# Optimization experiments

Hardware: AMD Instinct MI355X
Metric: run time of the kernel (lower is better)

Reference implementation:

```python
import jax, jax.numpy as jnp
import numpy as np

E = 256
H_HEADS = 8
HD = E // H_HEADS
NEG = -1e9


def setup_inputs() -> dict:
    key = jax.random.key(0)
    ks = jax.random.split(key, 16)
    B, Q, Hh, Ww = 16, 100, 64, 64
    S = Hh * Ww
    std = 1.0 / np.sqrt(E)
    inp = {
        "query_features": jax.random.normal(ks[0], (B, Q, E), jnp.float32),
        "image_features": jax.random.normal(ks[1], (B, E, Hh, Ww), jnp.float32),
        "mask": jax.random.randint(ks[2], (B, Q, Hh, Ww), 0, 2) > 0,
        "pos_query_embeddings": jax.random.normal(ks[3], (B, Q, E), jnp.float32),
        "pos_image_embeddings": jax.random.normal(ks[4], (B, S, E), jnp.float32),
        "Wq": jax.random.normal(ks[5], (E, E), jnp.float32) * std,
        "bq": jnp.zeros((E,), jnp.float32),
        "Wk": jax.random.normal(ks[6], (E, E), jnp.float32) * std,
        "bk": jnp.zeros((E,), jnp.float32),
        "Wv": jax.random.normal(ks[7], (E, E), jnp.float32) * std,
        "bv": jnp.zeros((E,), jnp.float32),
        "Wo": jax.random.normal(ks[8], (E, E), jnp.float32) * std,
        "bo": jnp.zeros((E,), jnp.float32),
    }
    return inp


def reference(query_features, image_features, mask, pos_query_embeddings,
              pos_image_embeddings, Wq, bq, Wk, bk, Wv, bv, Wo, bo):
    B, _, Hh, Ww = image_features.shape
    Q = query_features.shape[1]
    S = Hh * Ww
    # (B, S, E)
    img = jnp.transpose(image_features.reshape(B, E, S), (0, 2, 1))
    q = (query_features + pos_query_embeddings) @ Wq.T + bq  # (B,Q,E)
    k = (img + pos_image_embeddings) @ Wk.T + bk              # (B,S,E)
    v = img @ Wv.T + bv                                       # (B,S,E)
    q = q.reshape(B, Q, H_HEADS, HD).transpose(0, 2, 1, 3)    # (B,H,Q,D)
    k = k.reshape(B, S, H_HEADS, HD).transpose(0, 2, 1, 3)    # (B,H,S,D)
    v = v.reshape(B, S, H_HEADS, HD).transpose(0, 2, 1, 3)
    scale = 1.0 / jnp.sqrt(jnp.asarray(HD, q.dtype))
    scores = jnp.einsum('bhqd,bhsd->bhqs', q, k) * scale
    amask = mask.reshape(B, 1, Q, S)
    scores = jnp.where(amask, scores, NEG)
    attn = jax.nn.softmax(scores, axis=-1)
    out = jnp.einsum('bhqs,bhsd->bhqd', attn, v)
    out = out.transpose(0, 2, 1, 3).reshape(B, Q, E)
    return out @ Wo.T + bo
```

## Files before the change

### kernel.cpp

```cpp
#include <hip/hip_runtime.h>
#include <math.h>

#define BB 16
#define QQ 100
#define EE 256
#define NH 8
#define HD 32
#define SS 4096
#define QP 128
#define NZ 8
#define SCHUNK (SS / NZ)
#define M0 8.0f

typedef _Float16 half8_t __attribute__((ext_vector_type(8)));
typedef _Float16 half4_t __attribute__((ext_vector_type(4)));
typedef float floatx4 __attribute__((ext_vector_type(4)));

__global__ __launch_bounds__(256) void maskpack_kernel(
    const int* __restrict__ mask, unsigned* __restrict__ mbits)
{
    int gid  = blockIdx.x * 256 + threadIdx.x;
    int lane = gid & 63;
    int F    = gid & ~63;
    int s    = (F & (SS - 1)) + lane;
    int qp   = (F >> 12) & (QP - 1);
    int b    = F >> 19;
    int qc   = min(qp, QQ - 1);
    int v    = mask[((size_t)(b * QQ + qc)) * SS + s];
    unsigned long long bal = __ballot(v != 0);
    int w = (F & (SS - 1)) >> 5;
    if (lane == 0)
        mbits[((size_t)(b * (SS / 32) + w)) * QP + qp] = (unsigned)bal;
    if (lane == 32)
        mbits[((size_t)(b * (SS / 32) + w + 1)) * QP + qp] = (unsigned)(bal >> 32);
}

__global__ __launch_bounds__(256) void wcvt_kernel(
    const float* __restrict__ Wk, const float* __restrict__ Wv,
    _Float16* __restrict__ wk16a, _Float16* __restrict__ wv16a)
{
    int gid = blockIdx.x * 256 + threadIdx.x;
    int m = gid & 8191;
    const float* src = (gid < 8192) ? Wk : Wv;
    _Float16* dst = (gid < 8192) ? wk16a : wv16a;
    int li = m & 15, gg = (m >> 4) & 3, jj = (m >> 6) & 1;
    int kk = (m >> 7) & 7, w = (m >> 10) & 7;
    int e = w * 32 + jj * 16 + li;
    int f0 = kk * 32 + gg * 8;
    float4 a0 = *(const float4*)&src[(size_t)e * EE + f0];
    float4 a1 = *(const float4*)&src[(size_t)e * EE + f0 + 4];
    half8_t h;
    h[0]=(_Float16)a0.x; h[1]=(_Float16)a0.y; h[2]=(_Float16)a0.z; h[3]=(_Float16)a0.w;
    h[4]=(_Float16)a1.x; h[5]=(_Float16)a1.y; h[6]=(_Float16)a1.z; h[7]=(_Float16)a1.w;
    *(half8_t*)&dst[(size_t)m * 8] = h;
}

#define KV_STEP(KK, PC, PN, AKC, AVC)                                        \
  {                                                                          \
    float pv0 = PC[l * 33 + w4 + 0];                                         \
    float pv1 = PC[l * 33 + w4 + 1];                                         \
    float pv2 = PC[l * 33 + w4 + 2];                                         \
    float pv3 = PC[l * 33 + w4 + 3];                                         \
    half4_t hk, hv;                                                          \
    hv[0] = (_Float16)iv0; hk[0] = (_Float16)(iv0 + pv0);                    \
    hv[1] = (_Float16)iv1; hk[1] = (_Float16)(iv1 + pv1);                    \
    hv[2] = (_Float16)iv2; hk[2] = (_Float16)(iv2 + pv2);                    \
    hv[3] = (_Float16)iv3; hk[3] = (_Float16)(iv3 + pv3);                    \
    *(half4_t*)&AVC[l * 40 + w4] = hv;                                       \
    *(half4_t*)&AKC[l * 40 + w4] = hk;                                       \
    if ((KK) < 7) {                                                          \
      PN[pr * 33 + pc4 + 0] = pg.x;                                          \
      PN[pr * 33 + pc4 + 1] = pg.y;                                          \
      PN[pr * 33 + pc4 + 2] = pg.z;                                          \
      PN[pr * 33 + pc4 + 3] = pg.w;                                          \
    }                                                                        \
    __syncthreads();                                                         \
    if ((KK) < 6) pg = *(const float4*)(posb + ((KK) + 2) * 32);             \
    if ((KK) < 7) {                                                          \
      iv0 = imgb[(size_t)(((KK) + 1) * 32 + w4 + 0) * SS];                   \
      iv1 = imgb[(size_t)(((KK) + 1) * 32 + w4 + 1) * SS];                   \
      iv2 = imgb[(size_t)(((KK) + 1) * 32 + w4 + 2) * SS];                   \
      iv3 = imgb[(size_t)(((KK) + 1) * 32 + w4 + 3) * SS];                   \
    }                                                                        \
    half8_t wk0 = *(const half8_t*)(wkb + (KK) * 1024);                      \
    half8_t wk1 = *(const half8_t*)(wkb + (KK) * 1024 + 512);                \
    half8_t wv0 = *(const half8_t*)(wvb + (KK) * 1024);                      \
    half8_t wv1 = *(const half8_t*)(wvb + (KK) * 1024 + 512);                \
    half8_t afk0 = *(const half8_t*)&AKC[(0 * 16 + li) * 40 + gg * 8];       \
    half8_t afk1 = *(const half8_t*)&AKC[(1 * 16 + li) * 40 + gg * 8];       \
    half8_t afk2 = *(const half8_t*)&AKC[(2 * 16 + li) * 40 + gg * 8];       \
    half8_t afk3 = *(const half8_t*)&AKC[(3 * 16 + li) * 40 + gg * 8];       \
    acck[0][0] = __builtin_amdgcn_mfma_f32_16x16x32_f16(afk0, wk0, acck[0][0], 0, 0, 0); \
    acck[0][1] = __builtin_amdgcn_mfma_f32_16x16x32_f16(afk0, wk1, acck[0][1], 0, 0, 0); \
    acck[1][0] = __builtin_amdgcn_mfma_f32_16x16x32_f16(afk1, wk0, acck[1][0], 0, 0, 0); \
    acck[1][1] = __builtin_amdgcn_mfma_f32_16x16x32_f16(afk1, wk1, acck[1][1], 0, 0, 0); \
    acck[2][0] = __builtin_amdgcn_mfma_f32_16x16x32_f16(afk2, wk0, acck[2][0], 0, 0, 0); \
    acck[2][1] = __builtin_amdgcn_mfma_f32_16x16x32_f16(afk2, wk1, acck[2][1], 0, 0, 0); \
    acck[3][0] = __builtin_amdgcn_mfma_f32_16x16x32_f16(afk3, wk0, acck[3][0], 0, 0, 0); \
    acck[3][1] = __builtin_amdgcn_mfma_f32_16x16x32_f16(afk3, wk1, acck[3][1], 0, 0, 0); \
    half8_t afv0 = *(const half8_t*)&AVC[(0 * 16 + li) * 40 + gg * 8];       \
    half8_t afv1 = *(const half8_t*)&AVC[(1 * 16 + li) * 40 + gg * 8];       \
    half8_t afv2 = *(const half8_t*)&AVC[(2 * 16 + li) * 40 + gg * 8];       \
    half8_t afv3 = *(const half8_t*)&AVC[(3 * 16 + li) * 40 + gg * 8];       \
    accv[0][0] = __builtin_amdgcn_mfma_f32_16x16x32_f16(afv0, wv0, accv[0][0], 0, 0, 0); \
    accv[0][1] = __builtin_amdgcn_mfma_f32_16x16x32_f16(afv0, wv1, accv[0][1], 0, 0, 0); \
    accv[1][0] = __builtin_amdgcn_mfma_f32_16x16x32_f16(afv1, wv0, accv[1][0], 0, 0, 0); \
    accv[1][1] = __builtin_amdgcn_mfma_f32_16x16x32_f16(afv1, wv1, accv[1][1], 0, 0, 0); \
    accv[2][0] = __builtin_amdgcn_mfma_f32_16x16x32_f16(afv2, wv0, accv[2][0], 0, 0, 0); \
    accv[2][1] = __builtin_amdgcn_mfma_f32_16x16x32_f16(afv2, wv1, accv[2][1], 0, 0, 0); \
    accv[3][0] = __builtin_amdgcn_mfma_f32_16x16x32_f16(afv3, wv0, accv[3][0], 0, 0, 0); \
    accv[3][1] = __builtin_amdgcn_mfma_f32_16x16x32_f16(afv3, wv1, accv[3][1], 0, 0, 0); \
  }

__global__ __launch_bounds__(512, 2) void fused_kv_kernel(
    const float* __restrict__ img,
    const float* __restrict__ pos,
    const _Float16* __restrict__ wk16a, const float* __restrict__ bk,
    const _Float16* __restrict__ wv16a, const float* __restrict__ bv,
    _Float16* __restrict__ kbuf,
    _Float16* __restrict__ vt)
{
    __shared__ __align__(16) char smem_raw[37376];
    float* posT0 = (float*)smem_raw;
    float* posT1 = posT0 + 64 * 33;
    _Float16* A0k = (_Float16*)(posT1 + 64 * 33);
    _Float16* A0v = A0k + 2560;
    _Float16* A1k = A0v + 2560;
    _Float16* A1v = A1k + 2560;

    const int t  = threadIdx.x;
    const int w  = t >> 6, l = t & 63;
    const int gg = l >> 4, li = l & 15;
    const int pr = t >> 3, pc = t & 7;
    const int w4 = w * 4, pc4 = pc * 4;

    const int m0 = blockIdx.x * 64;
    const int b  = m0 >> 12;
    const int s0 = m0 & (SS - 1);

    const float* imgb = img + (size_t)b * EE * SS + s0 + l;
    const float* posb = pos + ((size_t)(b * SS + s0 + pr)) * EE + pc4;
    const _Float16* wkb = wk16a + ((size_t)(w * 16) * 64 + l) * 8;
    const _Float16* wvb = wv16a + ((size_t)(w * 16) * 64 + l) * 8;

    floatx4 acck[4][2] = {};
    floatx4 accv[4][2] = {};

    float4 pg = *(const float4*)posb;
    float iv0 = imgb[(size_t)(w4 + 0) * SS];
    float iv1 = imgb[(size_t)(w4 + 1) * SS];
    float iv2 = imgb[(size_t)(w4 + 2) * SS];
    float iv3 = imgb[(size_t)(w4 + 3) * SS];
    posT0[pr * 33 + pc4 + 0] = pg.x;
    posT0[pr * 33 + pc4 + 1] = pg.y;
    posT0[pr * 33 + pc4 + 2] = pg.z;
    posT0[pr * 33 + pc4 + 3] = pg.w;
    pg = *(const float4*)(posb + 32);
    __syncthreads();

    #pragma unroll 1
    for (int kp = 0; kp < 4; ++kp) {
        const int kk = kp * 2;
        KV_STEP(kk,     posT0, posT1, A0k, A0v)
        KV_STEP(kk + 1, posT1, posT0, A1k, A1v)
    }

    #pragma unroll
    for (int jj = 0; jj < 2; ++jj) {
        int e = w * 32 + jj * 16 + li;
        float bj = bk[e];
        #pragma unroll
        for (int i = 0; i < 4; ++i) {
            int row = m0 + i * 16 + gg * 4;
            #pragma unroll
            for (int r = 0; r < 4; ++r)
                kbuf[(size_t)(row + r) * EE + e] = (_Float16)(acck[i][jj][r] + bj);
        }
    }

    __syncthreads();
    _Float16* vstage = (_Float16*)smem_raw;
    #pragma unroll
    for (int jj = 0; jj < 2; ++jj) {
        int e_loc = w * 32 + jj * 16 + li;
        float bj = bv[e_loc];
        #pragma unroll
        for (int i = 0; i < 4; ++i) {
            int s_loc = i * 16 + gg * 4;
            half4_t h4;
            #pragma unroll
            for (int r = 0; r < 4; ++r)
                h4[r] = (_Float16)(accv[i][jj][r] + bj);
            *(half4_t*)&vstage[e_loc * 72 + s_loc] = h4;
        }
    }
    __syncthreads();
    #pragma unroll
    for (int c = 0; c < 4; ++c) {
        int row = c * 64 + (t >> 3);
        int so  = (t & 7) * 8;
        half8_t v8 = *(const half8_t*)&vstage[row * 72 + so];
        int hh = row >> 5, dd = row & 31;
        *(half8_t*)(vt + ((size_t)((b * NH + hh) * HD + dd)) * SS + s0 + so) = v8;
    }
}

__global__ __launch_bounds__(256) void proj_kernel(
    const float* __restrict__ x1, const float* __restrict__ x2,
    const float* __restrict__ W, const float* __restrict__ bias,
    float* __restrict__ outf, _Float16* __restrict__ out16,
    float oscale, int has_x2)
{
    const int row0 = blockIdx.x * 8;
    const int t = threadIdx.x;
    __shared__ float xs[8][256];

    #pragma unroll
    for (int p = 0; p < 8; ++p) {
        int idx = t + p * 256;
        int f = idx & 255, j = idx >> 8;
        size_t g = (size_t)(row0 + j) * EE + f;
        float v = x1[g];
        if (has_x2) v += x2[g];
        xs[j][f] = v;
    }
    __syncthreads();

    const int e = t;
    const float* wrow = W + (size_t)e * EE;
    float acc[8];
    const float bv = bias[e];
    #pragma unroll
    for (int j = 0; j < 8; ++j) acc[j] = bv;

    #pragma unroll 4
    for (int f4 = 0; f4 < 64; ++f4) {
        float4 w4 = *(const float4*)(wrow + f4 * 4);
        #pragma unroll
        for (int j = 0; j < 8; ++j) {
            float4 x4 = *(const float4*)&xs[j][f4 * 4];
            acc[j] = fmaf(w4.x, x4.x, acc[j]);
            acc[j] = fmaf(w4.y, x4.y, acc[j]);
            acc[j] = fmaf(w4.z, x4.z, acc[j]);
            acc[j] = fmaf(w4.w, x4.w, acc[j]);
        }
    }
    if (out16) {
        #pragma unroll
        for (int j = 0; j < 8; ++j)
            out16[(size_t)(row0 + j) * EE + e] = (_Float16)(acc[j] * oscale);
    } else {
        #pragma unroll
        for (int j = 0; j < 8; ++j)
            outf[(size_t)(row0 + j) * EE + e] = acc[j];
    }
}

__global__ __launch_bounds__(256) void attn_mfma_kernel(
    const _Float16* __restrict__ q16,
    const _Float16* __restrict__ kbuf,
    const _Float16* __restrict__ vt,
    const unsigned* __restrict__ mbits,
    float* __restrict__ part,
    float* __restrict__ pl)
{
    const int z = blockIdx.x, h = blockIdx.y, b = blockIdx.z;
    const int t = threadIdx.x;
    const int w = t >> 6, l = t & 63;
    const int g = l >> 4, li = l & 15;

    __shared__ _Float16 ks[64 * 40];
    __shared__ _Float16 vs[32 * 72];
    __shared__ _Float16 ps[128 * 72];
    __shared__ unsigned mw[2][QP];

    half8_t qf[2];
    {
        int q0r = min(32 * w + li, QQ - 1);
        int q1r = min(32 * w + 16 + li, QQ - 1);
        qf[0] = *(const half8_t*)(q16 + ((size_t)(b * QQ + q0r)) * EE + h * HD + g * 8);
        qf[1] = *(const half8_t*)(q16 + ((size_t)(b * QQ + q1r)) * EE + h * HD + g * 8);
    }

    float lsum[2][4] = {{0.f}};
    floatx4 accO[2][2] = {};

    for (int it = 0; it < SCHUNK / 64; ++it) {
        const int sblk = z * SCHUNK + it * 64;

        {
            int sl = t >> 2, koff = (t & 3) * 8;
            *(half8_t*)&ks[sl * 40 + koff] =
                *(const half8_t*)(kbuf + ((size_t)(b * SS + sblk + sl)) * EE + h * HD + koff);
            int dl = t >> 3, soff = (t & 7) * 8;
            *(half8_t*)&vs[dl * 72 + soff] =
                *(const half8_t*)(vt + ((size_t)((b * NH + h) * HD + dl)) * SS + sblk + soff);
            mw[t >> 7][t & 127] =
                mbits[((size_t)(b * (SS / 32) + (sblk >> 5) + (t >> 7))) * QP + (t & 127)];
        }
        __syncthreads();

        half8_t kf[4];
        #pragma unroll
        for (int st = 0; st < 4; ++st)
            kf[st] = *(const half8_t*)&ks[(st * 16 + li) * 40 + g * 8];
        floatx4 sc[2][4];
        #pragma unroll
        for (int qt = 0; qt < 2; ++qt)
            #pragma unroll
            for (int st = 0; st < 4; ++st) {
                floatx4 zero = {0.f, 0.f, 0.f, 0.f};
                sc[qt][st] = __builtin_amdgcn_mfma_f32_16x16x32_f16(
                    qf[qt], kf[st], zero, 0, 0, 0);
            }

        #pragma unroll
        for (int qt = 0; qt < 2; ++qt) {
            int qrow0 = 32 * w + qt * 16 + 4 * g;
            unsigned w0r[4], w1r[4];
            #pragma unroll
            for (int r = 0; r < 4; ++r) {
                w0r[r] = mw[0][qrow0 + r];
                w1r[r] = mw[1][qrow0 + r];
            }
            #pragma unroll
            for (int st = 0; st < 4; ++st)
                #pragma unroll
                for (int r = 0; r < 4; ++r) {
                    unsigned word = (st < 2) ? w0r[r] : w1r[r];
                    int keep = (word >> ((st & 1) * 16 + li)) & 1;
                    float pv = keep ? __expf(sc[qt][st][r] - M0) : 0.f;
                    _Float16 ph = (_Float16)pv;
                    lsum[qt][r] += (float)ph;
                    ps[(qrow0 + r) * 72 + st * 16 + li] = ph;
                }
        }

        half8_t vb[2][2];
        #pragma unroll
        for (int dt = 0; dt < 2; ++dt) {
            vb[dt][0] = *(const half8_t*)&vs[(dt * 16 + li) * 72 + g * 8];
            vb[dt][1] = *(const half8_t*)&vs[(dt * 16 + li) * 72 + 32 + g * 8];
        }
        #pragma unroll
        for (int qt = 0; qt < 2; ++qt) {
            half8_t a0 = *(const half8_t*)&ps[(32 * w + qt * 16 + li) * 72 + g * 8];
            half8_t a1 = *(const half8_t*)&ps[(32 * w + qt * 16 + li) * 72 + 32 + g * 8];
            #pragma unroll
            for (int dt = 0; dt < 2; ++dt) {
                accO[qt][dt] = __builtin_amdgcn_mfma_f32_16x16x32_f16(
                    a0, vb[dt][0], accO[qt][dt], 0, 0, 0);
                accO[qt][dt] = __builtin_amdgcn_mfma_f32_16x16x32_f16(
                    a1, vb[dt][1], accO[qt][dt], 0, 0, 0);
            }
        }
        __syncthreads();
    }

    #pragma unroll
    for (int qt = 0; qt < 2; ++qt)
        #pragma unroll
        for (int r = 0; r < 4; ++r) {
            float v = lsum[qt][r];
            v += __shfl_xor(v, 1, 64);
            v += __shfl_xor(v, 2, 64);
            v += __shfl_xor(v, 4, 64);
            v += __shfl_xor(v, 8, 64);
            lsum[qt][r] = v;
        }

    const size_t pbase = (((size_t)z * BB + b) * NH + h) * QP;
    #pragma unroll
    for (int qt = 0; qt < 2; ++qt) {
        int qrow0 = 32 * w + qt * 16 + 4 * g;
        #pragma unroll
        for (int r = 0; r < 4; ++r) {
            int qp = qrow0 + r;
            #pragma unroll
            for (int dt = 0; dt < 2; ++dt)
                part[(pbase + qp) * HD + dt * 16 + li] = accO[qt][dt][r];
            if (li == 0) pl[pbase + qp] = lsum[qt][r];
        }
    }
}

__global__ __launch_bounds__(256) void combine_kernel(
    const float* __restrict__ part, const float* __restrict__ pl,
    float* __restrict__ abuf)
{
    int tid = blockIdx.x * 256 + threadIdx.x;
    int d  = tid & 31;
    int qp = (tid >> 5) & 127;
    int h  = (tid >> 12) & 7;
    int b  = tid >> 15;
    if (qp >= QQ) return;
    float L = 0.f, O = 0.f;
    #pragma unroll
    for (int zz = 0; zz < NZ; ++zz) {
        size_t idx = (((size_t)zz * BB + b) * NH + h) * QP + qp;
        L += pl[idx];
        O += part[idx * HD + d];
    }
    abuf[((size_t)(b * QQ + qp)) * EE + h * HD + d] = O / fmaxf(L, 1e-30f);
}

extern "C" void kernel_launch(void* const* d_in, const int* in_sizes, int n_in,
                              void* d_out, int out_size, void* d_ws, size_t ws_size,
                              hipStream_t stream)
{
    const float* qf   = (const float*)d_in[0];
    const float* img  = (const float*)d_in[1];
    const int*   mask = (const int*)  d_in[2];
    const float* pq   = (const float*)d_in[3];
    const float* pimg = (const float*)d_in[4];
    const float* Wq   = (const float*)d_in[5];
    const float* bq   = (const float*)d_in[6];
    const float* Wk   = (const float*)d_in[7];
    const float* bk   = (const float*)d_in[8];
    const float* Wv   = (const float*)d_in[9];
    const float* bv   = (const float*)d_in[10];
    const float* Wo   = (const float*)d_in[11];
    const float* bo   = (const float*)d_in[12];
    float* out = (float*)d_out;

    const size_t MSE = (size_t)BB * SS * EE;

    _Float16* kbuf = (_Float16*)d_ws;
    _Float16* vtb  = kbuf + MSE;
    _Float16* q16  = vtb + MSE;
    unsigned* mbits = (unsigned*)(q16 + (size_t)BB * QQ * EE);
    float* part = (float*)(mbits + (size_t)BB * (SS / 32) * QP);
    float* pl   = part + (size_t)NZ * BB * NH * QP * HD;
    float* abuf = pl + (size_t)NZ * BB * NH * QP;
    _Float16* wk16a = (_Float16*)(abuf + (size_t)BB * QQ * EE);
    _Float16* wv16a = wk16a + (size_t)EE * EE;

    const float scale = 0.17677669529663687f;

    maskpack_kernel<<<(BB * QP * SS) / 256, 256, 0, stream>>>(mask, mbits);
    wcvt_kernel<<<64, 256, 0, stream>>>(Wk, Wv, wk16a, wv16a);
    proj_kernel<<<BB * QQ / 8, 256, 0, stream>>>(qf, pq, Wq, bq, nullptr, q16, scale, 1);
    fused_kv_kernel<<<BB * SS / 64, 512, 0, stream>>>(img, pimg, wk16a, bk, wv16a, bv, kbuf, vtb);
    attn_mfma_kernel<<<dim3(NZ, NH, BB), 256, 0, stream>>>(q16, kbuf, vtb, mbits, part, pl);
    combine_kernel<<<(BB * NH * QP * HD) / 256, 256, 0, stream>>>(part, pl, abuf);
    proj_kernel<<<BB * QQ / 8, 256, 0, stream>>>(abuf, nullptr, Wo, bo, out, nullptr, 1.f, 0);
}
```

Measured before the change: 305.0 us.

## Load K/V projection A-fragments directly from global, drop LDS staging loop

The fused K/V projection kernel no longer stages transposed image and position tiles through shared memory with double buffering and per-step barriers. Each wave now loads its own MFMA A-fragments straight from global memory and covers 16 rows by 128 output columns, which changes the per-wave tile shape and the fp16 weight layout to match. The main loop has no barriers, LDS use drops to the V staging buffer, and launch bounds request 4 blocks per CU. In exchange, image reads are strided per lane (one column per element), the same A data is loaded by two waves, and weight fragments are reread from global or cache each step.

```diff
diff --git a/kernel.cpp b/kernel.cpp
--- a/kernel.cpp
+++ b/kernel.cpp
@@ -43,10 +43,9 @@
     int m = gid & 8191;
     const float* src = (gid < 8192) ? Wk : Wv;
     _Float16* dst = (gid < 8192) ? wk16a : wv16a;
-    int li = m & 15, gg = (m >> 4) & 3, jj = (m >> 6) & 1;
-    int kk = (m >> 7) & 7, w = (m >> 10) & 7;
-    int e = w * 32 + jj * 16 + li;
-    int f0 = kk * 32 + gg * 8;
+    int l = m & 63, kk = (m >> 6) & 7, et = m >> 9;
+    int e = et * 16 + (l & 15);
+    int f0 = kk * 32 + (l >> 4) * 8;
     float4 a0 = *(const float4*)&src[(size_t)e * EE + f0];
     float4 a1 = *(const float4*)&src[(size_t)e * EE + f0 + 4];
     half8_t h;
@@ -55,64 +54,7 @@
     *(half8_t*)&dst[(size_t)m * 8] = h;
 }
 
-#define KV_STEP(KK, PC, PN, AKC, AVC)                                        \
-  {                                                                          \
-    float pv0 = PC[l * 33 + w4 + 0];                                         \
-    float pv1 = PC[l * 33 + w4 + 1];                                         \
-    float pv2 = PC[l * 33 + w4 + 2];                                         \
-    float pv3 = PC[l * 33 + w4 + 3];                                         \
-    half4_t hk, hv;                                                          \
-    hv[0] = (_Float16)iv0; hk[0] = (_Float16)(iv0 + pv0);                    \
-    hv[1] = (_Float16)iv1; hk[1] = (_Float16)(iv1 + pv1);                    \
-    hv[2] = (_Float16)iv2; hk[2] = (_Float16)(iv2 + pv2);                    \
-    hv[3] = (_Float16)iv3; hk[3] = (_Float16)(iv3 + pv3);                    \
-    *(half4_t*)&AVC[l * 40 + w4] = hv;                                       \
-    *(half4_t*)&AKC[l * 40 + w4] = hk;                                       \
-    if ((KK) < 7) {                                                          \
-      PN[pr * 33 + pc4 + 0] = pg.x;                                          \
-      PN[pr * 33 + pc4 + 1] = pg.y;                                          \
-      PN[pr * 33 + pc4 + 2] = pg.z;                                          \
-      PN[pr * 33 + pc4 + 3] = pg.w;                                          \
-    }                                                                        \
-    __syncthreads();                                                         \
-    if ((KK) < 6) pg = *(const float4*)(posb + ((KK) + 2) * 32);             \
-    if ((KK) < 7) {                                                          \
-      iv0 = imgb[(size_t)(((KK) + 1) * 32 + w4 + 0) * SS];                   \
-      iv1 = imgb[(size_t)(((KK) + 1) * 32 + w4 + 1) * SS];                   \
-      iv2 = imgb[(size_t)(((KK) + 1) * 32 + w4 + 2) * SS];                   \
-      iv3 = imgb[(size_t)(((KK) + 1) * 32 + w4 + 3) * SS];                   \
-    }                                                                        \
-    half8_t wk0 = *(const half8_t*)(wkb + (KK) * 1024);                      \
-    half8_t wk1 = *(const half8_t*)(wkb + (KK) * 1024 + 512);                \
-    half8_t wv0 = *(const half8_t*)(wvb + (KK) * 1024);                      \
-    half8_t wv1 = *(const half8_t*)(wvb + (KK) * 1024 + 512);                \
-    half8_t afk0 = *(const half8_t*)&AKC[(0 * 16 + li) * 40 + gg * 8];       \
-    half8_t afk1 = *(const half8_t*)&AKC[(1 * 16 + li) * 40 + gg * 8];       \
-    half8_t afk2 = *(const half8_t*)&AKC[(2 * 16 + li) * 40 + gg * 8];       \
-    half8_t afk3 = *(const half8_t*)&AKC[(3 * 16 + li) * 40 + gg * 8];       \
-    acck[0][0] = __builtin_amdgcn_mfma_f32_16x16x32_f16(afk0, wk0, acck[0][0], 0, 0, 0); \
-    acck[0][1] = __builtin_amdgcn_mfma_f32_16x16x32_f16(afk0, wk1, acck[0][1], 0, 0, 0); \
-    acck[1][0] = __builtin_amdgcn_mfma_f32_16x16x32_f16(afk1, wk0, acck[1][0], 0, 0, 0); \
-    acck[1][1] = __builtin_amdgcn_mfma_f32_16x16x32_f16(afk1, wk1, acck[1][1], 0, 0, 0); \
-    acck[2][0] = __builtin_amdgcn_mfma_f32_16x16x32_f16(afk2, wk0, acck[2][0], 0, 0, 0); \
-    acck[2][1] = __builtin_amdgcn_mfma_f32_16x16x32_f16(afk2, wk1, acck[2][1], 0, 0, 0); \
-    acck[3][0] = __builtin_amdgcn_mfma_f32_16x16x32_f16(afk3, wk0, acck[3][0], 0, 0, 0); \
-    acck[3][1] = __builtin_amdgcn_mfma_f32_16x16x32_f16(afk3, wk1, acck[3][1], 0, 0, 0); \
-    half8_t afv0 = *(const half8_t*)&AVC[(0 * 16 + li) * 40 + gg * 8];       \
-    half8_t afv1 = *(const half8_t*)&AVC[(1 * 16 + li) * 40 + gg * 8];       \
-    half8_t afv2 = *(const half8_t*)&AVC[(2 * 16 + li) * 40 + gg * 8];       \
-    half8_t afv3 = *(const half8_t*)&AVC[(3 * 16 + li) * 40 + gg * 8];       \
-    accv[0][0] = __builtin_amdgcn_mfma_f32_16x16x32_f16(afv0, wv0, accv[0][0], 0, 0, 0); \
-    accv[0][1] = __builtin_amdgcn_mfma_f32_16x16x32_f16(afv0, wv1, accv[0][1], 0, 0, 0); \
-    accv[1][0] = __builtin_amdgcn_mfma_f32_16x16x32_f16(afv1, wv0, accv[1][0], 0, 0, 0); \
-    accv[1][1] = __builtin_amdgcn_mfma_f32_16x16x32_f16(afv1, wv1, accv[1][1], 0, 0, 0); \
-    accv[2][0] = __builtin_amdgcn_mfma_f32_16x16x32_f16(afv2, wv0, accv[2][0], 0, 0, 0); \
-    accv[2][1] = __builtin_amdgcn_mfma_f32_16x16x32_f16(afv2, wv1, accv[2][1], 0, 0, 0); \
-    accv[3][0] = __builtin_amdgcn_mfma_f32_16x16x32_f16(afv3, wv0, accv[3][0], 0, 0, 0); \
-    accv[3][1] = __builtin_amdgcn_mfma_f32_16x16x32_f16(afv3, wv1, accv[3][1], 0, 0, 0); \
-  }
-
-__global__ __launch_bounds__(512, 2) void fused_kv_kernel(
+__global__ __launch_bounds__(512, 4) void fused_kv_kernel(
     const float* __restrict__ img,
     const float* __restrict__ pos,
     const _Float16* __restrict__ wk16a, const float* __restrict__ bk,
@@ -120,79 +62,77 @@
     _Float16* __restrict__ kbuf,
     _Float16* __restrict__ vt)
 {
-    __shared__ __align__(16) char smem_raw[37376];
-    float* posT0 = (float*)smem_raw;
-    float* posT1 = posT0 + 64 * 33;
-    _Float16* A0k = (_Float16*)(posT1 + 64 * 33);
-    _Float16* A0v = A0k + 2560;
-    _Float16* A1k = A0v + 2560;
-    _Float16* A1v = A1k + 2560;
+    __shared__ _Float16 vstage[256 * 72];
 
     const int t  = threadIdx.x;
     const int w  = t >> 6, l = t & 63;
     const int gg = l >> 4, li = l & 15;
-    const int pr = t >> 3, pc = t & 7;
-    const int w4 = w * 4, pc4 = pc * 4;
-
-    const int m0 = blockIdx.x * 64;
-    const int b  = m0 >> 12;
-    const int s0 = m0 & (SS - 1);
-
-    const float* imgb = img + (size_t)b * EE * SS + s0 + l;
-    const float* posb = pos + ((size_t)(b * SS + s0 + pr)) * EE + pc4;
-    const _Float16* wkb = wk16a + ((size_t)(w * 16) * 64 + l) * 8;
-    const _Float16* wvb = wv16a + ((size_t)(w * 16) * 64 + l) * 8;
-
-    floatx4 acck[4][2] = {};
-    floatx4 accv[4][2] = {};
-
-    float4 pg = *(const float4*)posb;
-    float iv0 = imgb[(size_t)(w4 + 0) * SS];
-    float iv1 = imgb[(size_t)(w4 + 1) * SS];
-    float iv2 = imgb[(size_t)(w4 + 2) * SS];
-    float iv3 = imgb[(size_t)(w4 + 3) * SS];
-    posT0[pr * 33 + pc4 + 0] = pg.x;
-    posT0[pr * 33 + pc4 + 1] = pg.y;
-    posT0[pr * 33 + pc4 + 2] = pg.z;
-    posT0[pr * 33 + pc4 + 3] = pg.w;
-    pg = *(const float4*)(posb + 32);
-    __syncthreads();
+    const int si = w & 3, eh = w >> 2;
+
+    const int m0  = blockIdx.x * 64;
+    const int b   = m0 >> 12;
+    const int s0  = m0 & (SS - 1);
+    const int ss0 = s0 + si * 16;
+    const int e0  = eh * 128;
+
+    const float* imgp = img + (size_t)b * EE * SS + (size_t)(gg * 8) * SS + ss0 + li;
+    const float* posp = pos + ((size_t)(b * SS + ss0 + li)) * EE + gg * 8;
+    const _Float16* wkp = wk16a + (size_t)eh * 32768 + l * 8;
+    const _Float16* wvp = wv16a + (size_t)eh * 32768 + l * 8;
+
+    floatx4 acck[8] = {};
+    floatx4 accv[8] = {};
 
     #pragma unroll 1
-    for (int kp = 0; kp < 4; ++kp) {
-        const int kk = kp * 2;
-        KV_STEP(kk,     posT0, posT1, A0k, A0v)
-        KV_STEP(kk + 1, posT1, posT0, A1k, A1v)
-    }
-
-    #pragma unroll
-    for (int jj = 0; jj < 2; ++jj) {
-        int e = w * 32 + jj * 16 + li;
+    for (int kk = 0; kk < 8; ++kk) {
+        const int f0 = kk * 32;
+
+        float iv[8];
+        #pragma unroll
+        for (int j = 0; j < 8; ++j)
+            iv[j] = imgp[(size_t)(f0 + j) * SS];
+        float4 p0 = *(const float4*)(posp + f0);
+        float4 p1 = *(const float4*)(posp + f0 + 4);
+
+        half8_t av8, ak8;
+        av8[0] = (_Float16)iv[0];  ak8[0] = (_Float16)(iv[0] + p0.x);
+        av8[1] = (_Float16)iv[1];  ak8[1] = (_Float16)(iv[1] + p0.y);
+        av8[2] = (_Float16)iv[2];  ak8[2] = (_Float16)(iv[2] + p0.z);
+        av8[3] = (_Float16)iv[3];  ak8[3] = (_Float16)(iv[3] + p0.w);
+        av8[4] = (_Float16)iv[4];  ak8[4] = (_Float16)(iv[4] + p1.x);
+        av8[5] = (_Float16)iv[5];  ak8[5] = (_Float16)(iv[5] + p1.y);
+        av8[6] = (_Float16)iv[6];  ak8[6] = (_Float16)(iv[6] + p1.z);
+        av8[7] = (_Float16)iv[7];  ak8[7] = (_Float16)(iv[7] + p1.w);
+
+        #pragma unroll
+        for (int n = 0; n < 8; ++n) {
+            half8_t wkf = *(const half8_t*)(wkp + (size_t)((n * 8 + kk) << 9));
+            half8_t wvf = *(const half8_t*)(wvp + (size_t)((n * 8 + kk) << 9));
+            acck[n] = __builtin_amdgcn_mfma_f32_16x16x32_f16(ak8, wkf, acck[n], 0, 0, 0);
+            accv[n] = __builtin_amdgcn_mfma_f32_16x16x32_f16(av8, wvf, accv[n], 0, 0, 0);
+        }
+    }
+
+    #pragma unroll
+    for (int n = 0; n < 8; ++n) {
+        int e = e0 + n * 16 + li;
         float bj = bk[e];
-        #pragma unroll
-        for (int i = 0; i < 4; ++i) {
-            int row = m0 + i * 16 + gg * 4;
-            #pragma unroll
-            for (int r = 0; r < 4; ++r)
-                kbuf[(size_t)(row + r) * EE + e] = (_Float16)(acck[i][jj][r] + bj);
-        }
-    }
-
-    __syncthreads();
-    _Float16* vstage = (_Float16*)smem_raw;
-    #pragma unroll
-    for (int jj = 0; jj < 2; ++jj) {
-        int e_loc = w * 32 + jj * 16 + li;
+        int row = b * SS + ss0 + gg * 4;
+        #pragma unroll
+        for (int r = 0; r < 4; ++r)
+            kbuf[(size_t)(row + r) * EE + e] = (_Float16)(acck[n][r] + bj);
+    }
+
+    #pragma unroll
+    for (int n = 0; n < 8; ++n) {
+        int e_loc = e0 + n * 16 + li;
         float bj = bv[e_loc];
-        #pragma unroll
-        for (int i = 0; i < 4; ++i) {
-            int s_loc = i * 16 + gg * 4;
-            half4_t h4;
-            #pragma unroll
-            for (int r = 0; r < 4; ++r)
-                h4[r] = (_Float16)(accv[i][jj][r] + bj);
-            *(half4_t*)&vstage[e_loc * 72 + s_loc] = h4;
-        }
+        int s_loc = si * 16 + gg * 4;
+        half4_t h4;
+        #pragma unroll
+        for (int r = 0; r < 4; ++r)
+            h4[r] = (_Float16)(accv[n][r] + bj);
+        *(half4_t*)&vstage[e_loc * 72 + s_loc] = h4;
     }
     __syncthreads();
     #pragma unroll
```

Result: slower. 349.2 us (+14.5%).
